# Performance work log

Hardware: AMD Instinct MI355X
Metric: run time of the kernel (lower is better)

Reference implementation:

```python
import jax, jax.numpy as jnp
import numpy as np

VOCAB = 50257
EMBED_DIM = 768


def setup_inputs() -> dict:
    key = jax.random.key(0)
    k1, k2 = jax.random.split(key)
    x = jax.random.randint(k1, (8, 2048), 0, VOCAB, dtype=jnp.int64 if jax.config.jax_enable_x64 else jnp.int32)
    weight = jax.random.normal(k2, (EMBED_DIM, VOCAB), dtype=jnp.float32)
    return {"x": x, "weight": weight}


def reference(x, weight):
    # Original: one_hot(x, vocab) @ weight.T  ==  gather rows of weight.T
    # weight: [embed_dim, vocab]; output: [batch, seq, embed_dim]
    return jnp.take(weight.T, x, axis=0)
```

## Files before the change

kernel.cpp:

```cpp
#include <hip/hip_runtime.h>


#define VOCAB 50257
#define EMBED 768
#define WINB 32
#define NWIN 1571
#define RG 4
#define ROWS 192
#define LSTRIDE 33
#define CAP 64

__device__ __forceinline__ int xcd_swizzle(int bid, int nwg) {
  const int NX = 8;
  int q = nwg / NX, r = nwg % NX;
  int xcd = bid % NX, idx = bid / NX;
  int base = (xcd < r) ? xcd * (q + 1) : r * (q + 1) + (xcd - r) * q;
  return base + idx;
}

__global__ __launch_bounds__(256) void scatter_kernel(const int* __restrict__ x,
                                                      int* __restrict__ cur,
                                                      int* __restrict__ buckets,
                                                      int* __restrict__ spill_cnt,
                                                      int* __restrict__ spill,
                                                      int n) {
  int i = blockIdx.x * blockDim.x + threadIdx.x;
  if (i < n) {
    int v = x[i];
    int win = v >> 5;
    int p = atomicAdd(&cur[win], 1);
    if (p < CAP) {
      buckets[win * CAP + p] = (i << 5) | (v & 31);
    } else {
      int s = atomicAdd(spill_cnt, 1);
      spill[s] = (i << 16) | v;
    }
  }
}

__global__ __launch_bounds__(256) void gather_kernel(const float* __restrict__ w,
                                                     const int* __restrict__ cur,
                                                     const int* __restrict__ buckets,
                                                     float* __restrict__ out) {
  __shared__ float lds[ROWS * LSTRIDE];
  __shared__ int toks[CAP];
  const int logical = xcd_swizzle(blockIdx.x, NWIN * RG);
  const int wid = logical % NWIN;
  const int rg  = logical / NWIN;
  const int row0 = rg * ROWS;
  const int col0 = wid * WINB;
  const int tid = threadIdx.x;
  const int wave = tid >> 6, lane = tid & 63;

  int m = cur[wid];
  if (m > CAP) m = CAP;

  if (tid < m) toks[tid] = buckets[wid * CAP + tid];

  if (wid != NWIN - 1) {
    #pragma unroll
    for (int j = tid; j < ROWS * 8; j += 256) {
      int r = j >> 3, c4 = (j & 7) << 2;
      float4 v = *(const float4*)&w[(size_t)(row0 + r) * VOCAB + col0 + c4];
      float* d = &lds[r * LSTRIDE + c4];
      d[0] = v.x; d[1] = v.y; d[2] = v.z; d[3] = v.w;
    }
  } else {
    for (int j = tid; j < ROWS * 8; j += 256) {
      int r = j >> 3, c4 = (j & 7) << 2;
      float* d = &lds[r * LSTRIDE + c4];
      for (int u = 0; u < 4; ++u) {
        int c = col0 + c4 + u;
        d[u] = (c < VOCAB) ? w[(size_t)(row0 + r) * VOCAB + c] : 0.f;
      }
    }
  }
  __syncthreads();

  for (int i = wave; i < m; i += 4) {
    int pk = toks[i];
    int t = pk >> 5, c = pk & 31;
    float* o = &out[(size_t)t * EMBED + row0];
    #pragma unroll
    for (int k = 0; k < 3; ++k)
      __builtin_nontemporal_store(lds[(k * 64 + lane) * LSTRIDE + c],
                                  &o[k * 64 + lane]);
  }
}

__global__ __launch_bounds__(256) void spill_kernel(const float* __restrict__ w,
                                                    const int* __restrict__ spill_cnt,
                                                    const int* __restrict__ spill,
                                                    float* __restrict__ out) {
  int cnt = *spill_cnt;
  for (int s = blockIdx.x; s < cnt; s += gridDim.x) {
    int pk = spill[s];
    int t = pk >> 16, v = pk & 0xFFFF;
    for (int e = threadIdx.x; e < EMBED; e += 256)
      out[(size_t)t * EMBED + e] = w[(size_t)e * VOCAB + v];
  }
}

extern "C" void kernel_launch(void* const* d_in, const int* in_sizes, int n_in,
                              void* d_out, int out_size, void* d_ws, size_t ws_size,
                              hipStream_t stream) {
  const int*   x = (const int*)d_in[0];
  const float* w = (const float*)d_in[1];
  float* out = (float*)d_out;
  const int n = in_sizes[0];

  int* cur       = (int*)d_ws;
  int* spill_cnt = cur + NWIN;
  int* spill     = spill_cnt + 1;
  int* buckets   = spill + n;

  hipMemsetAsync(cur, 0, (NWIN + 1) * sizeof(int), stream);
  scatter_kernel<<<(n + 255) / 256, 256, 0, stream>>>(x, cur, buckets,
                                                      spill_cnt, spill, n);
  gather_kernel<<<NWIN * RG, 256, 0, stream>>>(w, cur, buckets, out);
  spill_kernel<<<64, 256, 0, stream>>>(w, spill_cnt, spill, out);
}
```

Baseline: 49.63 us.

## Fuse spill pass into gather kernel and halve rows per block

Removes the separate spill kernel launch by running the spill loop in the first 64 blocks of the gather kernel. Row groups double to 8 with 96 rows each, which gives more, smaller blocks. LDS writes become float4 stores with a padded stride of 36, and the XCD swizzle drops its remainder handling because the grid now divides evenly by 8. A fused spill write could race with gather writes only for different tokens, so it stays correct while saving one launch plus its tail.

```diff
diff --git a/kernel.cpp b/kernel.cpp
--- a/kernel.cpp
+++ b/kernel.cpp
@@ -5,17 +5,16 @@
 #define EMBED 768
 #define WINB 32
 #define NWIN 1571
-#define RG 4
-#define ROWS 192
-#define LSTRIDE 33
+#define RG 8
+#define ROWS 96
+#define LSTRIDE 36
 #define CAP 64
 
 __device__ __forceinline__ int xcd_swizzle(int bid, int nwg) {
   const int NX = 8;
-  int q = nwg / NX, r = nwg % NX;
+  int q = nwg / NX;
   int xcd = bid % NX, idx = bid / NX;
-  int base = (xcd < r) ? xcd * (q + 1) : r * (q + 1) + (xcd - r) * q;
-  return base + idx;
+  return xcd * q + idx;
 }
 
 __global__ __launch_bounds__(256) void scatter_kernel(const int* __restrict__ x,
@@ -41,6 +40,8 @@
 __global__ __launch_bounds__(256) void gather_kernel(const float* __restrict__ w,
                                                      const int* __restrict__ cur,
                                                      const int* __restrict__ buckets,
+                                                     const int* __restrict__ spill_cnt,
+                                                     const int* __restrict__ spill,
                                                      float* __restrict__ out) {
   __shared__ float lds[ROWS * LSTRIDE];
   __shared__ int toks[CAP];
@@ -59,20 +60,23 @@
 
   if (wid != NWIN - 1) {
     #pragma unroll
-    for (int j = tid; j < ROWS * 8; j += 256) {
-      int r = j >> 3, c4 = (j & 7) << 2;
-      float4 v = *(const float4*)&w[(size_t)(row0 + r) * VOCAB + col0 + c4];
-      float* d = &lds[r * LSTRIDE + c4];
-      d[0] = v.x; d[1] = v.y; d[2] = v.z; d[3] = v.w;
+    for (int k = 0; k < 3; ++k) {
+      int j = k * 256 + tid;
+      int r = j >> 3, g = j & 7;
+      float4 v = *(const float4*)&w[(size_t)(row0 + r) * VOCAB + col0 + (g << 2)];
+      *(float4*)&lds[r * LSTRIDE + (g << 2)] = v;
     }
   } else {
-    for (int j = tid; j < ROWS * 8; j += 256) {
-      int r = j >> 3, c4 = (j & 7) << 2;
-      float* d = &lds[r * LSTRIDE + c4];
+    for (int k = 0; k < 3; ++k) {
+      int j = k * 256 + tid;
+      int r = j >> 3, g = j & 7;
+      float4 v;
+      float* pv = (float*)&v;
       for (int u = 0; u < 4; ++u) {
-        int c = col0 + c4 + u;
-        d[u] = (c < VOCAB) ? w[(size_t)(row0 + r) * VOCAB + c] : 0.f;
+        int c = col0 + (g << 2) + u;
+        pv[u] = (c < VOCAB) ? w[(size_t)(row0 + r) * VOCAB + c] : 0.f;
       }
+      *(float4*)&lds[r * LSTRIDE + (g << 2)] = v;
     }
   }
   __syncthreads();
@@ -81,23 +85,19 @@
     int pk = toks[i];
     int t = pk >> 5, c = pk & 31;
     float* o = &out[(size_t)t * EMBED + row0];
-    #pragma unroll
-    for (int k = 0; k < 3; ++k)
-      __builtin_nontemporal_store(lds[(k * 64 + lane) * LSTRIDE + c],
-                                  &o[k * 64 + lane]);
+    __builtin_nontemporal_store(lds[lane * LSTRIDE + c], &o[lane]);
+    if (lane < ROWS - 64)
+      __builtin_nontemporal_store(lds[(64 + lane) * LSTRIDE + c], &o[64 + lane]);
   }
-}
 
-__global__ __launch_bounds__(256) void spill_kernel(const float* __restrict__ w,
-                                                    const int* __restrict__ spill_cnt,
-                                                    const int* __restrict__ spill,
-                                                    float* __restrict__ out) {
-  int cnt = *spill_cnt;
-  for (int s = blockIdx.x; s < cnt; s += gridDim.x) {
-    int pk = spill[s];
-    int t = pk >> 16, v = pk & 0xFFFF;
-    for (int e = threadIdx.x; e < EMBED; e += 256)
-      out[(size_t)t * EMBED + e] = w[(size_t)e * VOCAB + v];
+  if (blockIdx.x < 64) {
+    int cnt = *spill_cnt;
+    for (int s = blockIdx.x; s < cnt; s += 64) {
+      int pk = spill[s];
+      int t = pk >> 16, v = pk & 0xFFFF;
+      for (int e = tid; e < EMBED; e += 256)
+        out[(size_t)t * EMBED + e] = w[(size_t)e * VOCAB + v];
+    }
   }
 }
 
@@ -117,6 +117,6 @@
   hipMemsetAsync(cur, 0, (NWIN + 1) * sizeof(int), stream);
   scatter_kernel<<<(n + 255) / 256, 256, 0, stream>>>(x, cur, buckets,
                                                       spill_cnt, spill, n);
-  gather_kernel<<<NWIN * RG, 256, 0, stream>>>(w, cur, buckets, out);
-  spill_kernel<<<64, 256, 0, stream>>>(w, spill_cnt, spill, out);
+  gather_kernel<<<NWIN * RG, 256, 0, stream>>>(w, cur, buckets,
+                                               spill_cnt, spill, out);
 }
```

New measurement: 46.78 us. 1.06x faster.
